# Kernel tuning notes

Hardware: AMD Instinct MI355X
Metric: run time of the kernel (lower is better)

Reference implementation:

```python
import jax, jax.numpy as jnp
import numpy as np
import math
from jax import lax

B, L, D, P, V, K = 4, 2048, 512, 128, 8, 4


def _lin(x, w, b):
    # torch Linear: y = x @ W^T + b, W shape (out, in)
    return jnp.einsum('...i,oi->...o', x, w) + b


def _gelu(v):
    return jax.nn.gelu(v, approximate=False)


def _dwconv_causal(x_ncl, w, b):
    # depthwise causal conv: torch Conv1d(groups=D, padding=K-1) then [:, :, :L]
    y = lax.conv_general_dilated(x_ncl, w, (1,), [(K - 1, 0)],
                                 dimension_numbers=('NCH', 'OIH', 'NCH'),
                                 feature_group_count=D)
    return y + b[None, :, None]


def _ln(v, g, b):
    m = v.mean(-1, keepdims=True)
    var = v.var(-1, keepdims=True)
    return (v - m) / jnp.sqrt(var + 1e-5) * g + b


def setup_inputs() -> dict:
    key = jax.random.key(0)
    it = iter(jax.random.split(key, 64))
    def nrm(shape, s=0.02):
        return jax.random.normal(next(it), shape, dtype=jnp.float32) * s
    z = lambda *s: jnp.zeros(s, jnp.float32)
    return dict(
        x=nrm((B, L, D), 1.0),
        lc_w=nrm((D, 1, K)), lc_b=z(D),
        cg_w=nrm((D, 1, K)), cg_b=z(D),
        cp_w=nrm((D, D)), cp_b=z(D),
        tw_w=nrm((D, D)), tw_b=z(D),
        omega_scale=jnp.full((D,), 0.01, jnp.float32),
        pi0_w=nrm((D, D)), pi0_b=z(D),
        pi2_w=nrm((D, D)), pi2_b=z(D),
        m1v_w=nrm((D, D)), m1v_b=z(D),
        m1o_w=nrm((D, D)), m1o_b=z(D),
        mag_w=nrm((D, D)), mag_b=z(D),
        mag_scale=jnp.asarray(5.0, jnp.float32),
        qo_w=nrm((D, D)), qo_b=z(D),
        ke_w=nrm((P, D)), ke_b=z(P),
        ve_w=nrm((V, D)), ve_b=z(V),
        sk0_w=nrm((D, 2 * D)), sk0_b=z(D),
        sk2_w=nrm((P, D)), sk2_b=z(P),
        sg_w=nrm((1, D)), sg_b=z(1),
        kvo_w=nrm((D, V)), kvo_b=z(D),
        ln_g=jnp.ones(5 * D, jnp.float32), ln_b=z(5 * D),
        o1_w=nrm((2 * D, 5 * D)), o1_b=z(2 * D),
        o2_w=nrm((D, 2 * D)), o2_b=z(D),
    )


def reference(x, lc_w, lc_b, cg_w, cg_b, cp_w, cp_b, tw_w, tw_b, omega_scale,
              pi0_w, pi0_b, pi2_w, pi2_b, m1v_w, m1v_b, m1o_w, m1o_b,
              mag_w, mag_b, mag_scale, qo_w, qo_b, ke_w, ke_b, ve_w, ve_b,
              sk0_w, sk0_b, sk2_w, sk2_b, sg_w, sg_b, kvo_w, kvo_b,
              ln_g, ln_b, o1_w, o1_b, o2_w, o2_b):
    Bs, Ls, Ds = x.shape
    # local gated causal depthwise conv branch
    xc = jnp.transpose(x, (0, 2, 1))                          # (B, D, L)
    co = _dwconv_causal(xc, lc_w, lc_b)
    cg = jax.nn.sigmoid(_dwconv_causal(xc, cg_w, cg_b))
    conv_out = _lin(jnp.transpose(co * cg, (0, 2, 1)), cp_w, cp_b)
    # evolving phases
    omega_scaled = _lin(x, tw_w, tw_b) * jnp.abs(omega_scale)
    phi = _lin(_gelu(_lin(x, pi0_w, pi0_b)), pi2_w, pi2_b) + jnp.cumsum(omega_scaled, axis=1)
    cos_phi = jnp.cos(phi)
    sin_phi = jnp.sin(phi)
    # magnitude-weighted phase memory
    v1 = _lin(x, m1v_w, m1v_b)
    magnitude = jax.nn.sigmoid(_lin(x, mag_w, mag_b)) * jnp.abs(mag_scale)
    wv1 = magnitude * v1
    sqrt_mag = jnp.sqrt(jnp.cumsum(magnitude, axis=1) + 1e-8)
    mem1_cos = jnp.cumsum(wv1 * cos_phi, axis=1) / sqrt_mag
    mem1_sin = jnp.cumsum(wv1 * sin_phi, axis=1) / sqrt_mag
    phi_q = phi + _lin(x, qo_w, qo_b)
    pos_ret = (mem1_cos * jnp.cos(phi_q) + mem1_sin * jnp.sin(phi_q)) / math.sqrt(Ds)
    pos_out = _lin(pos_ret, m1o_w, m1o_b)
    # phase-keyed associative KV memory
    query_phase = jnp.tanh(_lin(x, ke_w, ke_b)) * math.pi    # (B, L, P)
    values = _lin(x, ve_w, ve_b)                              # (B, L, V)
    store_gate = jax.nn.sigmoid(_lin(x, sg_w, sg_b))          # (B, L, 1)
    positions = jnp.arange(1, Ls + 1, dtype=x.dtype).reshape(1, -1, 1)
    context_avg = jnp.cumsum(x, axis=1) / positions
    storage_phase = jnp.tanh(_lin(_gelu(_lin(jnp.concatenate([x, context_avg], -1), sk0_w, sk0_b)), sk2_w, sk2_b)) * math.pi
    gated_vals = values * store_gate                          # (B, L, V)
    kv_mem_cos = jnp.cumsum(jnp.cos(storage_phase)[..., None] * gated_vals[:, :, None, :], axis=1)
    kv_mem_sin = jnp.cumsum(jnp.sin(storage_phase)[..., None] * gated_vals[:, :, None, :], axis=1)
    gate_norm = jnp.sqrt(jnp.maximum(jnp.cumsum(store_gate, axis=1), 1.0))[..., None]  # (B, L, 1, 1)
    kv_mem_cos = kv_mem_cos / gate_norm
    kv_mem_sin = kv_mem_sin / gate_norm
    kv_retrieved = (jnp.cos(query_phase)[..., None] * kv_mem_cos +
                    jnp.sin(query_phase)[..., None] * kv_mem_sin).sum(axis=2) / math.sqrt(P)
    kv_out = _lin(kv_retrieved, kvo_w, kvo_b)
    # combine (dropout is identity in eval)
    combined = jnp.concatenate([conv_out, pos_out, kv_out, x * cos_phi, x * sin_phi], axis=-1)
    h = _ln(combined, ln_g, ln_b)
    h = _lin(_gelu(_lin(h, o1_w, o1_b)), o2_w, o2_b)
    return x + h
```

## Files before the change

### kernel.cpp

```cpp
#include <hip/hip_runtime.h>
#include <cstdint>

typedef unsigned short u16;
typedef short short8 __attribute__((ext_vector_type(8)));
typedef float floatx4 __attribute__((ext_vector_type(4)));

#define B_ 4
#define L_ 2048
#define D_ 512
#define P_ 128
#define V_ 8
#define BL (B_ * L_)
#define NC_ 128
#define CH_ 16
#define PI_F 3.14159265358979323846f

__device__ inline u16 f2b(float f) {
    unsigned u = __float_as_uint(f);
    unsigned r = u + 0x7FFFu + ((u >> 16) & 1u);
    return (u16)(r >> 16);
}
__device__ inline float b2f(u16 h) {
    return __uint_as_float(((unsigned)h) << 16);
}
__device__ inline float gelu_f(float v) {
    return 0.5f * v * (1.0f + erff(v * 0.70710678118654752f));
}
__device__ inline float sigm(float v) {
    return 1.0f / (1.0f + __expf(-v));
}
__device__ inline float tanh_fast(float v) {
    return 1.0f - 2.0f / (1.0f + __expf(2.0f * v));
}

__device__ inline void async16(const u16* g, u16* l) {
    __builtin_amdgcn_global_load_lds(
        (const __attribute__((address_space(1))) unsigned int*)g,
        (__attribute__((address_space(3))) unsigned int*)l, 16, 0, 0);
}

extern __shared__ u16 smem_dyn[];

enum { EPI_F32 = 0, EPI_BF16 = 1, EPI_GELU_BF16 = 2, EPI_RESID_F32 = 3,
       EPI_PASS1 = 4, EPI_ATOMIC = 5 };

template <int EPI>
__device__ __forceinline__ void gemm_body(
    const u16* __restrict__ A, int lda,
    const u16* __restrict__ W, int ldw,
    const float* __restrict__ bias,
    void* __restrict__ Cout, int ldc, int N, int K,
    const float* __restrict__ resid, int mt, int nt)
{
    const int tid  = threadIdx.x;
    const int lane = tid & 63;
    const int wid  = tid >> 6;
    const int wm   = wid & 1, wn = wid >> 1;
    const int l16  = lane & 15, quad = lane >> 4;
    const int rswz = (l16 >> 1) & 3;

    floatx4 acc[4][4] = {};

    const u16* Ab = A + (size_t)(mt * 128) * lda;
    const u16* Wb = W + (size_t)(nt * 128) * ldw;

    const int srow = lane >> 2;
    const int scol = ((lane & 3) ^ ((srow >> 1) & 3)) * 8;
    const u16* ga0 = Ab + (size_t)(wid * 16 + srow) * lda + scol;
    const u16* ga1 = Ab + (size_t)(64 + wid * 16 + srow) * lda + scol;
    const u16* gb0 = Wb + (size_t)(wid * 16 + srow) * ldw + scol;
    const u16* gb1 = Wb + (size_t)(64 + wid * 16 + srow) * ldw + scol;

    const int lA0 = (wid * 16) * 32;
    const int lA1 = (64 + wid * 16) * 32;

    const int nsteps = K >> 5;

    auto stage = [&](int t, int s) {
        u16* base = smem_dyn + s * 8192;
        const int ko = t * 32;
        async16(ga0 + ko, base + lA0);
        async16(ga1 + ko, base + lA1);
        async16(gb0 + ko, base + 4096 + lA0);
        async16(gb1 + ko, base + 4096 + lA1);
    };

    auto readfrag = [&](int slot, short8 (&a)[4], short8 (&b)[4]) {
        const u16* As = smem_dyn + slot * 8192;
        const u16* Bs = As + 4096;
#pragma unroll
        for (int i = 0; i < 4; i++)
            a[i] = *(const short8*)(&As[(wm * 64 + i * 16 + l16) * 32 + (quad ^ rswz) * 8]);
#pragma unroll
        for (int j = 0; j < 4; j++)
            b[j] = *(const short8*)(&Bs[(wn * 64 + j * 16 + l16) * 32 + (quad ^ rswz) * 8]);
    };

    auto mfma16 = [&](short8 (&a)[4], short8 (&b)[4]) {
        __builtin_amdgcn_s_setprio(1);
#pragma unroll
        for (int i = 0; i < 4; i++)
#pragma unroll
            for (int j = 0; j < 4; j++)
                acc[i][j] = __builtin_amdgcn_mfma_f32_16x16x32_bf16(a[i], b[j], acc[i][j], 0, 0, 0);
        __builtin_amdgcn_s_setprio(0);
    };

    stage(0, 0);
    if (nsteps > 1) stage(1, 1);
    if (nsteps > 2) stage(2, 2);
    if (nsteps > 2)      asm volatile("s_waitcnt vmcnt(8)" ::: "memory");
    else if (nsteps > 1) asm volatile("s_waitcnt vmcnt(4)" ::: "memory");
    else                 asm volatile("s_waitcnt vmcnt(0)" ::: "memory");
    __builtin_amdgcn_s_barrier();
    asm volatile("" ::: "memory");

    short8 aE[4], bE[4], aO[4], bO[4];
    readfrag(0, aE, bE);

    for (int t = 0; t < nsteps; t += 2) {
        asm volatile("s_waitcnt lgkmcnt(0)" ::: "memory");
        if (t + 2 < nsteps)      asm volatile("s_waitcnt vmcnt(4)" ::: "memory");
        else if (t + 1 < nsteps) asm volatile("s_waitcnt vmcnt(0)" ::: "memory");
        __builtin_amdgcn_s_barrier();
        asm volatile("" ::: "memory");
        if (t + 3 < nsteps) stage(t + 3, t % 3);
        if (t + 1 < nsteps) readfrag((t + 1) % 3, aO, bO);
        mfma16(aE, bE);
        const int t1 = t + 1;
        asm volatile("s_waitcnt lgkmcnt(0)" ::: "memory");
        if (t1 + 2 < nsteps)      asm volatile("s_waitcnt vmcnt(4)" ::: "memory");
        else if (t1 + 1 < nsteps) asm volatile("s_waitcnt vmcnt(0)" ::: "memory");
        __builtin_amdgcn_s_barrier();
        asm volatile("" ::: "memory");
        if (t1 + 3 < nsteps) stage(t1 + 3, t1 % 3);
        if (t1 + 1 < nsteps) readfrag((t1 + 1) % 3, aE, bE);
        mfma16(aO, bO);
    }

#pragma unroll
    for (int i = 0; i < 4; i++) {
#pragma unroll
        for (int j = 0; j < 4; j++) {
#pragma unroll
            for (int r = 0; r < 4; r++) {
                int grow = mt * 128 + wm * 64 + i * 16 + quad * 4 + r;
                int gcol = nt * 128 + wn * 64 + j * 16 + l16;
                if (gcol < N) {
                    float v = acc[i][j][r] + (bias ? bias[gcol] : 0.0f);
                    size_t off = (size_t)grow * ldc + gcol;
                    if (EPI == EPI_F32)            ((float*)Cout)[off] = v;
                    else if (EPI == EPI_BF16)      ((u16*)Cout)[off] = f2b(v);
                    else if (EPI == EPI_GELU_BF16) ((u16*)Cout)[off] = f2b(gelu_f(v));
                    else if (EPI == EPI_PASS1) {
                        float vv = (gcol >= 512 && gcol < 1024) ? gelu_f(v) : v;
                        ((u16*)Cout)[off] = f2b(vv);
                    }
                    else if (EPI == EPI_RESID_F32) ((float*)Cout)[off] = v + resid[off];
                    else                           atomicAdd(&((float*)Cout)[off], v);
                }
            }
        }
    }
}

template <int EPI>
__global__ __launch_bounds__(256)
void gemm256(const u16* __restrict__ A, int lda,
             const u16* __restrict__ W, int ldw,
             const float* __restrict__ bias,
             void* __restrict__ C, int ldc, int N, int K,
             const float* __restrict__ resid)
{
    int kz = blockIdx.z;
    gemm_body<EPI>(A + (size_t)kz * K, lda, W + (size_t)kz * K, ldw,
                   kz == 0 ? bias : nullptr, C, ldc, N, K, resid,
                   blockIdx.x, blockIdx.y);
}

__global__ __launch_bounds__(256)
void mega1(const u16* __restrict__ xcat, const u16* __restrict__ convg,
           const u16* __restrict__ wcat1, const float* __restrict__ bcat1,
           const u16* __restrict__ kesgw, const float* __restrict__ kesgb,
           const u16* __restrict__ cpw, const float* __restrict__ cp_b,
           u16* __restrict__ out1, float* __restrict__ kesgo, u16* __restrict__ combined)
{
    int y = blockIdx.y, mt = blockIdx.x;
    if (y < 20)
        gemm_body<EPI_PASS1>(xcat, 1024, wcat1, 512, bcat1, out1, 2560, 2560, 512, nullptr, mt, y);
    else if (y < 22)
        gemm_body<EPI_F32>(xcat, 1024, kesgw, 512, kesgb, kesgo, 144, 144, 512, nullptr, mt, y - 20);
    else
        gemm_body<EPI_BF16>(convg, 512, cpw, 512, cp_b, combined, 2560, 512, 512, nullptr, mt, y - 22);
}

__global__ __launch_bounds__(256)
void mega2(const u16* __restrict__ posret, const u16* __restrict__ xcat,
           const u16* __restrict__ m1ow, const float* __restrict__ m1o_b,
           const u16* __restrict__ sk0w, const float* __restrict__ sk0_b,
           u16* __restrict__ combined, u16* __restrict__ sk0g)
{
    int y = blockIdx.y, mt = blockIdx.x;
    if (y < 4)
        gemm_body<EPI_BF16>(posret, 512, m1ow, 512, m1o_b, combined + 512, 2560, 512, 512, nullptr, mt, y);
    else
        gemm_body<EPI_GELU_BF16>(xcat, 1024, sk0w, 1024, sk0_b, sk0g, 512, 512, 1024, nullptr, mt, y - 4);
}

__global__ __launch_bounds__(256)
void prep_weights(const float* tw, const float* pi0, const float* m1v, const float* mag, const float* qo,
                  const float* ke, const float* ve, const float* sg,
                  const float* pi2, const float* cp, const float* sk0, const float* sk2,
                  const float* m1o, const float* o1, const float* o2,
                  const float* tw_b, const float* pi0_b, const float* m1v_b, const float* mag_b, const float* qo_b,
                  const float* ke_b, const float* ve_b, const float* sg_b,
                  u16* wcat1, float* bcat1, u16* kesgw, float* kesgb,
                  u16* pi2w, u16* cpw, u16* sk0w, u16* sk2w, u16* m1ow, u16* o1w, u16* o2w)
{
    int idx = blockIdx.x * 256 + threadIdx.x;
    const int n0 = 2560 * 512;
    const int n1 = n0 + 256 * 512;
    const int n2 = n1 + 512 * 512;
    const int n3 = n2 + 512 * 512;
    const int n4 = n3 + 512 * 1024;
    const int n5 = n4 + 128 * 512;
    const int n6 = n5 + 512 * 512;
    const int n7 = n6 + 1024 * 2560;
    const int n8 = n7 + 512 * 1024;
    const int n9 = n8 + 2560;
    const int n10 = n9 + 256;
    if (idx < n0) {
        int r = idx >> 9, k = idx & 511;
        const float* s = (r < 512) ? tw : (r < 1024) ? pi0 : (r < 1536) ? m1v : (r < 2048) ? mag : qo;
        wcat1[idx] = f2b(s[(r & 511) * 512 + k]);
    } else if (idx < n1) {
        int i = idx - n0; int r = i >> 9, k = i & 511;
        float v;
        if (r < 128)      v = ke[r * 512 + k];
        else if (r < 136) v = ve[(r - 128) * 512 + k];
        else if (r == 136) v = sg[k];
        else               v = 0.0f;
        kesgw[i] = f2b(v);
    }
    else if (idx < n2) { int i = idx - n1; pi2w[i] = f2b(pi2[i]); }
    else if (idx < n3) { int i = idx - n2; cpw[i]  = f2b(cp[i]); }
    else if (idx < n4) { int i = idx - n3; sk0w[i] = f2b(sk0[i]); }
    else if (idx < n5) { int i = idx - n4; sk2w[i] = f2b(sk2[i]); }
    else if (idx < n6) { int i = idx - n5; m1ow[i] = f2b(m1o[i]); }
    else if (idx < n7) { int i = idx - n6; o1w[i]  = f2b(o1[i]); }
    else if (idx < n8) { int i = idx - n7; o2w[i]  = f2b(o2[i]); }
    else if (idx < n9) {
        int i = idx - n8;
        const float* s = (i < 512) ? tw_b : (i < 1024) ? pi0_b : (i < 1536) ? m1v_b : (i < 2048) ? mag_b : qo_b;
        bcat1[i] = s[i & 511];
    } else if (idx < n10) {
        int i = idx - n9;
        kesgb[i] = (i < 128) ? ke_b[i] : (i < 136) ? ve_b[i - 128] : (i == 136) ? sg_b[0] : 0.0f;
    }
}

__global__ __launch_bounds__(256)
void conv_gate(const float* __restrict__ x,
               const float* __restrict__ lcw, const float* __restrict__ lcb,
               const float* __restrict__ cgw, const float* __restrict__ cgb,
               u16* __restrict__ out, u16* __restrict__ xcat)
{
    int idx = blockIdx.x * 256 + threadIdx.x;
    int d = idx & 511; int bl = idx >> 9;
    int l = bl & (L_ - 1); int b = bl >> 11;
    float a0 = 0.f, a1 = 0.f, xv3 = 0.f;
#pragma unroll
    for (int k = 0; k < 4; k++) {
        int ls = l - 3 + k;
        if (ls >= 0) {
            float xv = x[((size_t)(b * L_ + ls)) * 512 + d];
            if (k == 3) xv3 = xv;
            a0 += xv * lcw[d * 4 + k];
            a1 += xv * cgw[d * 4 + k];
        }
    }
    a0 += lcb[d];
    a1 = sigm(a1 + cgb[d]);
    out[idx] = f2b(a0 * a1);
    xcat[(size_t)bl * 1024 + d] = f2b(xv3);
}

__device__ __forceinline__ void scan_a_body(
    int blk, const u16* __restrict__ out1, const float* __restrict__ x,
    const float* __restrict__ oscale, const float* __restrict__ msc,
    float* __restrict__ cs_o, float* __restrict__ cs_x, float* __restrict__ cs_m)
{
    int nc = blk & 15, dt = (blk >> 4) & 7, b = blk >> 7;
    int t = threadIdx.x; int dl = t & 63, lg = t >> 6;
    int d = dt * 64 + dl;
    float os = fabsf(oscale[d]);
    float ms = fabsf(msc[0]);
    float so = 0.f, sx = 0.f, sm = 0.f;
    int l0 = nc * 128 + lg * 32;
    for (int i = 0; i < 32; i++) {
        size_t r = (size_t)(b * L_ + l0 + i);
        so += b2f(out1[r * 2560 + d]) * os;
        sm += sigm(b2f(out1[r * 2560 + 1536 + d])) * ms;
        sx += x[r * 512 + d];
    }
    __shared__ float sh[3][4][64];
    sh[0][lg][dl] = so; sh[1][lg][dl] = sx; sh[2][lg][dl] = sm;
    __syncthreads();
    if (t < 64) {
        float a = 0.f, xx = 0.f, m = 0.f;
        for (int g = 0; g < 4; g++) { a += sh[0][g][t]; xx += sh[1][g][t]; m += sh[2][g][t]; }
        size_t o = ((size_t)(b * 16 + nc)) * 512 + dt * 64 + t;
        cs_o[o] = a; cs_x[o] = xx; cs_m[o] = m;
    }
}

__device__ __forceinline__ void gate_body(const float* __restrict__ kesgo,
                                          float* __restrict__ gni)
{
    int b = threadIdx.x >> 6; int lane = threadIdx.x & 63;
    float v[32]; float s = 0.f;
#pragma unroll
    for (int i = 0; i < 32; i++) {
        int l = lane * 32 + i;
        v[i] = sigm(kesgo[((size_t)(b * L_ + l)) * 144 + 136]);
        s += v[i];
    }
    float sc = s;
#pragma unroll
    for (int ofs = 1; ofs < 64; ofs <<= 1) {
        float t = __shfl_up(sc, ofs, 64);
        if (lane >= ofs) sc += t;
    }
    float run = sc - s;
#pragma unroll
    for (int i = 0; i < 32; i++) {
        run += v[i];
        gni[b * L_ + lane * 32 + i] = rsqrtf(fmaxf(run, 1.0f));
    }
}

__global__ __launch_bounds__(256)
void stage2(const u16* __restrict__ out1, const u16* __restrict__ pi2w,
            const float* __restrict__ pi2_b, u16* __restrict__ phib,
            const float* __restrict__ x, const float* __restrict__ oscale,
            const float* __restrict__ msc,
            float* __restrict__ cs_o, float* __restrict__ cs_x, float* __restrict__ cs_m,
            const float* __restrict__ kesgo, float* __restrict__ gni)
{
    int blk = blockIdx.x;
    if (blk < 256)
        gemm_body<EPI_BF16>(out1 + 512, 2560, pi2w, 512, pi2_b, phib, 512, 512, 512,
                            nullptr, blk & 63, blk >> 6);
    else if (blk < 768)
        scan_a_body(blk - 256, out1, x, oscale, msc, cs_o, cs_x, cs_m);
    else
        gate_body(kesgo, gni);
}

__global__ __launch_bounds__(256)
void scan_c(const u16* __restrict__ out1, const u16* __restrict__ phib,
            const float* __restrict__ oscale, const float* __restrict__ msc,
            const float* __restrict__ cs_o,
            float* __restrict__ phi, float* __restrict__ cs_wc, float* __restrict__ cs_ws)
{
    int blk = blockIdx.x;
    int nc = blk & 15, dt = (blk >> 4) & 7, b = blk >> 7;
    int t = threadIdx.x; int dl = t & 63, lg = t >> 6;
    int d = dt * 64 + dl;
    float os = fabsf(oscale[d]);
    float ms = fabsf(msc[0]);
    int l0 = nc * 128 + lg * 32;
    float so = 0.f;
    for (int i = 0; i < 32; i++) {
        size_t r = (size_t)(b * L_ + l0 + i);
        so += b2f(out1[r * 2560 + d]) * os;
    }
    __shared__ float sh[4][64];
    __shared__ float shw[2][4][64];
    sh[lg][dl] = so;
    __syncthreads();
    float pre = 0.f;
    for (int p = 0; p < nc; p++) pre += cs_o[((size_t)(b * 16 + p)) * 512 + d];
    for (int g = 0; g < lg; g++) pre += sh[g][dl];
    float cum = pre, swc = 0.f, sws = 0.f;
    for (int i = 0; i < 32; i++) {
        size_t r = (size_t)(b * L_ + l0 + i);
        cum += b2f(out1[r * 2560 + d]) * os;
        float ph = b2f(phib[r * 512 + d]) + cum;
        phi[r * 512 + d] = ph;
        float mg = sigm(b2f(out1[r * 2560 + 1536 + d])) * ms;
        float wv = mg * b2f(out1[r * 2560 + 1024 + d]);
        float s = __sinf(ph), c = __cosf(ph);
        swc += wv * c; sws += wv * s;
    }
    shw[0][lg][dl] = swc; shw[1][lg][dl] = sws;
    __syncthreads();
    if (t < 64) {
        float a = 0.f, bb = 0.f;
        for (int g = 0; g < 4; g++) { a += shw[0][g][t]; bb += shw[1][g][t]; }
        size_t o = ((size_t)(b * 16 + nc)) * 512 + dt * 64 + t;
        cs_wc[o] = a; cs_ws[o] = bb;
    }
}

__global__ __launch_bounds__(256)
void scan_e(const u16* __restrict__ out1, const float* __restrict__ phi,
            const float* __restrict__ x, const float* __restrict__ msc,
            const float* __restrict__ cs_m, const float* __restrict__ cs_x,
            const float* __restrict__ cs_wc, const float* __restrict__ cs_ws,
            u16* __restrict__ posret, u16* __restrict__ xcat, u16* __restrict__ combined)
{
    int blk = blockIdx.x;
    int nc = blk & 15, dt = (blk >> 4) & 7, b = blk >> 7;
    int t = threadIdx.x; int dl = t & 63, lg = t >> 6;
    int d = dt * 64 + dl;
    float ms = fabsf(msc[0]);
    int l0 = nc * 128 + lg * 32;
    float sm = 0.f, swc = 0.f, sws = 0.f, sx = 0.f;
    for (int i = 0; i < 32; i++) {
        size_t r = (size_t)(b * L_ + l0 + i);
        float ph = phi[r * 512 + d];
        float mg = sigm(b2f(out1[r * 2560 + 1536 + d])) * ms;
        float wv = mg * b2f(out1[r * 2560 + 1024 + d]);
        float s = __sinf(ph), c = __cosf(ph);
        sm += mg; swc += wv * c; sws += wv * s; sx += x[r * 512 + d];
    }
    __shared__ float sh[4][4][64];
    sh[0][lg][dl] = sm; sh[1][lg][dl] = swc; sh[2][lg][dl] = sws; sh[3][lg][dl] = sx;
    __syncthreads();
    float cm = 0.f, cwc = 0.f, cws = 0.f, cx = 0.f;
    for (int p = 0; p < nc; p++) {
        size_t o = ((size_t)(b * 16 + p)) * 512 + d;
        cm += cs_m[o]; cwc += cs_wc[o]; cws += cs_ws[o]; cx += cs_x[o];
    }
    for (int g = 0; g < lg; g++) {
        cm += sh[0][g][dl]; cwc += sh[1][g][dl]; cws += sh[2][g][dl]; cx += sh[3][g][dl];
    }
    const float invsqD = 0.044194173824159216f;
    for (int i = 0; i < 32; i++) {
        int l = l0 + i;
        size_t r = (size_t)(b * L_ + l);
        float ph = phi[r * 512 + d];
        float mg = sigm(b2f(out1[r * 2560 + 1536 + d])) * ms;
        float wv = mg * b2f(out1[r * 2560 + 1024 + d]);
        float xv = x[r * 512 + d];
        float s = __sinf(ph), c = __cosf(ph);
        cm += mg; cwc += wv * c; cws += wv * s; cx += xv;
        float smag = sqrtf(cm + 1e-8f);
        float m1c = cwc / smag, m1s = cws / smag;
        float phq = ph + b2f(out1[r * 2560 + 2048 + d]);
        float sq = __sinf(phq), cq = __cosf(phq);
        float pr = (m1c * cq + m1s * sq) * invsqD;
        posret[r * 512 + d] = f2b(pr);
        xcat[r * 1024 + 512 + d] = f2b(cx / (float)(l + 1));
        combined[r * 2560 + 1536 + d] = f2b(xv * c);
        combined[r * 2560 + 2048 + d] = f2b(xv * s);
    }
}

__global__ __launch_bounds__(64)
void kv_chunk(const float* __restrict__ sppre, const float* __restrict__ kesgo,
              float* __restrict__ spc, float* __restrict__ sps,
              float* __restrict__ csum)
{
    int blk = blockIdx.x; int nc = blk & (NC_ - 1), b = blk >> 7;
    int t = threadIdx.x;
    float Sc[2][8] = {}, Ss[2][8] = {};
    for (int i = 0; i < CH_; i++) {
        size_t r = (size_t)(b * L_ + nc * CH_ + i);
        float sgate = sigm(kesgo[r * 144 + 136]);
        float g[8];
#pragma unroll
        for (int v = 0; v < 8; v++) g[v] = kesgo[r * 144 + 128 + v] * sgate;
#pragma unroll
        for (int j = 0; j < 2; j++) {
            int p = t + j * 64;
            float sp = tanh_fast(sppre[r * 128 + p]) * PI_F;
            float s = __sinf(sp), c = __cosf(sp);
            spc[r * 128 + p] = c; sps[r * 128 + p] = s;
#pragma unroll
            for (int v = 0; v < 8; v++) { Sc[j][v] += c * g[v]; Ss[j][v] += s * g[v]; }
        }
    }
    size_t base = (size_t)blk * 2048;
#pragma unroll
    for (int j = 0; j < 2; j++)
#pragma unroll
        for (int v = 0; v < 8; v++) {
            csum[base + (t + j * 64) * 8 + v]        = Sc[j][v];
            csum[base + 1024 + (t + j * 64) * 8 + v] = Ss[j][v];
        }
}

__global__ __launch_bounds__(256)
void kv_scan(const float* __restrict__ cin, float* __restrict__ cex)
{
    int t = blockIdx.x * 256 + threadIdx.x;
    int pv = t & 1023; int cs = (t >> 10) & 1; int b = t >> 11;
    float run = 0.f;
    for (int nc = 0; nc < NC_; nc++) {
        size_t o = ((size_t)(b * NC_ + nc)) * 2048 + cs * 1024 + pv;
        cex[o] = run; run += cin[o];
    }
}

__global__ __launch_bounds__(64)
void kv_retrieve(const float* __restrict__ spc, const float* __restrict__ sps,
                 const float* __restrict__ kesgo,
                 const float* __restrict__ gni, const float* __restrict__ cex,
                 const float* __restrict__ kvo_w, const float* __restrict__ kvo_b,
                 u16* __restrict__ combined)
{
    int blk = blockIdx.x; int nc = blk & (NC_ - 1), b = blk >> 7;
    int t = threadIdx.x;
    const int nb = t * 8;
    float wr[8][8], br[8];
#pragma unroll
    for (int n = 0; n < 8; n++) {
        *(float4*)&wr[n][0] = *(const float4*)&kvo_w[(nb + n) * 8];
        *(float4*)&wr[n][4] = *(const float4*)&kvo_w[(nb + n) * 8 + 4];
        br[n] = kvo_b[nb + n];
    }
    float Sc[2][8], Ss[2][8];
    size_t base = (size_t)blk * 2048;
#pragma unroll
    for (int j = 0; j < 2; j++)
#pragma unroll
        for (int v = 0; v < 8; v++) {
            Sc[j][v] = cex[base + (t + j * 64) * 8 + v];
            Ss[j][v] = cex[base + 1024 + (t + j * 64) * 8 + v];
        }
    for (int i = 0; i < CH_; i++) {
        size_t r = (size_t)(b * L_ + nc * CH_ + i);
        float sgate = sigm(kesgo[r * 144 + 136]);
        float g[8];
#pragma unroll
        for (int v = 0; v < 8; v++) g[v] = kesgo[r * 144 + 128 + v] * sgate;
        float part[8];
#pragma unroll
        for (int v = 0; v < 8; v++) part[v] = 0.f;
#pragma unroll
        for (int j = 0; j < 2; j++) {
            int p = t + j * 64;
            float c = spc[r * 128 + p], s = sps[r * 128 + p];
#pragma unroll
            for (int v = 0; v < 8; v++) { Sc[j][v] += c * g[v]; Ss[j][v] += s * g[v]; }
            float qp = tanh_fast(kesgo[r * 144 + p]) * PI_F;
            float sq = __sinf(qp), cq = __cosf(qp);
#pragma unroll
            for (int v = 0; v < 8; v++) part[v] += cq * Sc[j][v] + sq * Ss[j][v];
        }
#pragma unroll
        for (int ofs = 1; ofs < 64; ofs <<= 1)
#pragma unroll
            for (int v = 0; v < 8; v++) part[v] += __shfl_xor(part[v], ofs, 64);
        float scale = gni[r] * 0.08838834764831845f;
        float pv[8];
#pragma unroll
        for (int v = 0; v < 8; v++) pv[v] = part[v] * scale;
        u16 outv[8];
#pragma unroll
        for (int n = 0; n < 8; n++) {
            float a = br[n];
#pragma unroll
            for (int v = 0; v < 8; v++) a += pv[v] * wr[n][v];
            outv[n] = f2b(a);
        }
        *(uint4*)&combined[r * 2560 + 1024 + nb] = *(const uint4*)outv;
    }
}

__global__ __launch_bounds__(320)
void ln_rows(u16* __restrict__ combined, const float* __restrict__ g, const float* __restrict__ bb)
{
    size_t m = blockIdx.x; int t = threadIdx.x;
    u16 vv[8];
    *(uint4*)vv = *(const uint4*)&combined[m * 2560 + t * 8];
    float f[8]; float s = 0.f, s2 = 0.f;
#pragma unroll
    for (int k = 0; k < 8; k++) { f[k] = b2f(vv[k]); s += f[k]; s2 += f[k] * f[k]; }
#pragma unroll
    for (int ofs = 1; ofs < 64; ofs <<= 1) {
        s  += __shfl_xor(s, ofs, 64);
        s2 += __shfl_xor(s2, ofs, 64);
    }
    __shared__ float shs[5], shs2[5];
    int wv = t >> 6;
    if ((t & 63) == 0) { shs[wv] = s; shs2[wv] = s2; }
    __syncthreads();
    float S = 0.f, S2 = 0.f;
#pragma unroll
    for (int i = 0; i < 5; i++) { S += shs[i]; S2 += shs2[i]; }
    float mean = S * (1.0f / 2560.0f);
    float var  = S2 * (1.0f / 2560.0f) - mean * mean;
    float rstd = rsqrtf(var + 1e-5f);
#pragma unroll
    for (int k = 0; k < 8; k++) {
        int c = t * 8 + k;
        vv[k] = f2b((f[k] - mean) * rstd * g[c] + bb[c]);
    }
    *(uint4*)&combined[m * 2560 + t * 8] = *(const uint4*)vv;
}

extern "C" void kernel_launch(void* const* d_in, const int* in_sizes, int n_in,
                              void* d_out, int out_size, void* d_ws, size_t ws_size,
                              hipStream_t stream)
{
    const float* x     = (const float*)d_in[0];
    const float* lc_w  = (const float*)d_in[1];
    const float* lc_b  = (const float*)d_in[2];
    const float* cg_w  = (const float*)d_in[3];
    const float* cg_b  = (const float*)d_in[4];
    const float* cp_w  = (const float*)d_in[5];
    const float* cp_b  = (const float*)d_in[6];
    const float* tw_w  = (const float*)d_in[7];
    const float* tw_b  = (const float*)d_in[8];
    const float* omega_scale = (const float*)d_in[9];
    const float* pi0_w = (const float*)d_in[10];
    const float* pi0_b = (const float*)d_in[11];
    const float* pi2_w = (const float*)d_in[12];
    const float* pi2_b = (const float*)d_in[13];
    const float* m1v_w = (const float*)d_in[14];
    const float* m1v_b = (const float*)d_in[15];
    const float* m1o_w = (const float*)d_in[16];
    const float* m1o_b = (const float*)d_in[17];
    const float* mag_w = (const float*)d_in[18];
    const float* mag_b = (const float*)d_in[19];
    const float* mag_scale = (const float*)d_in[20];
    const float* qo_w  = (const float*)d_in[21];
    const float* qo_b  = (const float*)d_in[22];
    const float* ke_w  = (const float*)d_in[23];
    const float* ke_b  = (const float*)d_in[24];
    const float* ve_w  = (const float*)d_in[25];
    const float* ve_b  = (const float*)d_in[26];
    const float* sk0_w = (const float*)d_in[27];
    const float* sk0_b = (const float*)d_in[28];
    const float* sk2_w = (const float*)d_in[29];
    const float* sk2_b = (const float*)d_in[30];
    const float* sg_w  = (const float*)d_in[31];
    const float* sg_b  = (const float*)d_in[32];
    const float* kvo_w = (const float*)d_in[33];
    const float* kvo_b = (const float*)d_in[34];
    const float* ln_g  = (const float*)d_in[35];
    const float* ln_b  = (const float*)d_in[36];
    const float* o1_w  = (const float*)d_in[37];
    const float* o1_b  = (const float*)d_in[38];
    const float* o2_w  = (const float*)d_in[39];
    const float* o2_b  = (const float*)d_in[40];
    float* out = (float*)d_out;

    char* base = (char*)d_ws;
    size_t off = 0;
    auto alloc = [&](size_t bytes) -> void* {
        void* p = base + off;
        off += (bytes + 255) & ~(size_t)255;
        return p;
    };

    u16*   wcat1  = (u16*)  alloc((size_t)2560 * 512 * 2);
    float* bcat1  = (float*)alloc(2560 * 4);
    u16*   kesgw  = (u16*)  alloc((size_t)256 * 512 * 2);
    float* kesgb  = (float*)alloc(256 * 4);
    u16*   pi2w   = (u16*)  alloc((size_t)512 * 512 * 2);
    u16*   cpw    = (u16*)  alloc((size_t)512 * 512 * 2);
    u16*   sk0w   = (u16*)  alloc((size_t)512 * 1024 * 2);
    u16*   sk2w   = (u16*)  alloc((size_t)128 * 512 * 2);
    u16*   m1ow   = (u16*)  alloc((size_t)512 * 512 * 2);
    u16*   o1w    = (u16*)  alloc((size_t)1024 * 2560 * 2);
    u16*   o2w    = (u16*)  alloc((size_t)512 * 1024 * 2);
    u16*   xcat   = (u16*)  alloc((size_t)BL * 1024 * 2);
    u16*   out1   = (u16*)  alloc((size_t)BL * 2560 * 2);
    u16*   phib   = (u16*)  alloc((size_t)BL * 512 * 2);
    float* phi    = (float*)alloc((size_t)BL * 512 * 4);
    float* kesgo  = (float*)alloc((size_t)BL * 144 * 4);
    u16*   convg  = (u16*)  alloc((size_t)BL * 512 * 2);
    float* sppre  = (float*)alloc((size_t)BL * 128 * 4);
    u16*   combined = (u16*)alloc((size_t)BL * 2560 * 2);
    float* cs_o   = (float*)alloc((size_t)4 * 16 * 512 * 4);
    float* cs_x   = (float*)alloc((size_t)4 * 16 * 512 * 4);
    float* cs_m   = (float*)alloc((size_t)4 * 16 * 512 * 4);
    float* cs_wc  = (float*)alloc((size_t)4 * 16 * 512 * 4);
    float* cs_ws  = (float*)alloc((size_t)4 * 16 * 512 * 4);
    float* gni    = (float*)alloc((size_t)BL * 4);
    u16*   posret = convg;
    u16*   sk0g   = out1;
    float* spc    = phi;
    float* sps    = phi + (size_t)BL * 128;
    float* kvcs   = (float*)phib;
    float* kvex   = (float*)phib + (size_t)B_ * NC_ * 2048;
    u16*   o1g    = xcat;
    (void)ws_size; (void)in_sizes; (void)n_in; (void)out_size;

    const size_t SMEM = 49152;

    prep_weights<<<23307, 256, 0, stream>>>(
        tw_w, pi0_w, m1v_w, mag_w, qo_w, ke_w, ve_w, sg_w,
        pi2_w, cp_w, sk0_w, sk2_w, m1o_w, o1_w, o2_w,
        tw_b, pi0_b, m1v_b, mag_b, qo_b, ke_b, ve_b, sg_b,
        wcat1, bcat1, kesgw, kesgb, pi2w, cpw, sk0w, sk2w, m1ow, o1w, o2w);
    conv_gate<<<16384, 256, 0, stream>>>(x, lc_w, lc_b, cg_w, cg_b, convg, xcat);
    mega1<<<dim3(64, 26), 256, SMEM, stream>>>(xcat, convg, wcat1, bcat1,
                                               kesgw, kesgb, cpw, cp_b,
                                               out1, kesgo, combined);
    stage2<<<769, 256, SMEM, stream>>>(out1, pi2w, pi2_b, phib,
                                       x, omega_scale, mag_scale,
                                       cs_o, cs_x, cs_m, kesgo, gni);
    scan_c<<<512, 256, 0, stream>>>(out1, phib, omega_scale, mag_scale, cs_o,
                                    phi, cs_wc, cs_ws);
    scan_e<<<512, 256, 0, stream>>>(out1, phi, x, mag_scale, cs_m, cs_x, cs_wc, cs_ws,
                                    posret, xcat, combined);
    mega2<<<dim3(64, 8), 256, SMEM, stream>>>(posret, xcat, m1ow, m1o_b,
                                              sk0w, sk0_b, combined, sk0g);
    hipMemsetAsync(sppre, 0, (size_t)BL * 128 * 4, stream);
    gemm256<EPI_ATOMIC><<<dim3(64, 1, 4), 256, SMEM, stream>>>(sk0g, 512, sk2w, 512, sk2_b,
                                                               sppre, 128, 128, 128, nullptr);
    kv_chunk<<<4 * NC_, 64, 0, stream>>>(sppre, kesgo, spc, sps, kvcs);
    kv_scan<<<32, 256, 0, stream>>>(kvcs, kvex);
    kv_retrieve<<<4 * NC_, 64, 0, stream>>>(spc, sps, kesgo, gni, kvex, kvo_w, kvo_b, combined);
    ln_rows<<<8192, 320, 0, stream>>>(combined, ln_g, ln_b);
    gemm256<EPI_GELU_BF16><<<dim3(64, 8), 256, SMEM, stream>>>(combined, 2560, o1w, 2560, o1_b,
                                                               o1g, 1024, 1024, 2560, nullptr);
    gemm256<EPI_RESID_F32><<<dim3(64, 4), 256, SMEM, stream>>>(o1g, 1024, o2w, 1024, o2_b,
                                                               out, 512, 512, 1024, x);
}
```

Measured before the change: 560.4 us.

## Give each wave private LDS A tiles and load B fragments directly from global

Restructures the GEMM main loop so each wave stages only its own 64-row A slice into a private triple-buffered LDS region, while the weight (B) fragments are read straight from global memory into registers. This drops the workgroup-wide s_barrier calls between pipeline steps, since no LDS is shared across waves anymore. In exchange, A rows shared by waves with the same wm are loaded twice, and B is fetched from global/L2 with per-lane strided loads instead of coalesced shared staging. The vmcnt accounting now mixes async LDS loads with register loads, which adds ordering risk.

```diff
diff --git a/kernel.cpp b/kernel.cpp
--- a/kernel.cpp
+++ b/kernel.cpp
@@ -61,41 +61,44 @@
 
     floatx4 acc[4][4] = {};
 
-    const u16* Ab = A + (size_t)(mt * 128) * lda;
-    const u16* Wb = W + (size_t)(nt * 128) * ldw;
+    const u16* Ab = A + (size_t)(mt * 128 + wm * 64) * lda;
+    const u16* Wb = W + (size_t)(nt * 128 + wn * 64) * ldw;
 
     const int srow = lane >> 2;
     const int scol = ((lane & 3) ^ ((srow >> 1) & 3)) * 8;
-    const u16* ga0 = Ab + (size_t)(wid * 16 + srow) * lda + scol;
-    const u16* ga1 = Ab + (size_t)(64 + wid * 16 + srow) * lda + scol;
-    const u16* gb0 = Wb + (size_t)(wid * 16 + srow) * ldw + scol;
-    const u16* gb1 = Wb + (size_t)(64 + wid * 16 + srow) * ldw + scol;
-
-    const int lA0 = (wid * 16) * 32;
-    const int lA1 = (64 + wid * 16) * 32;
-
+    const u16* gA0 = Ab + (size_t)(srow)      * lda + scol;
+    const u16* gA1 = Ab + (size_t)(16 + srow) * lda + scol;
+    const u16* gA2 = Ab + (size_t)(32 + srow) * lda + scol;
+    const u16* gA3 = Ab + (size_t)(48 + srow) * lda + scol;
+    const u16* gB0 = Wb + (size_t)(l16)      * ldw + quad * 8;
+    const u16* gB1 = Wb + (size_t)(16 + l16) * ldw + quad * 8;
+    const u16* gB2 = Wb + (size_t)(32 + l16) * ldw + quad * 8;
+    const u16* gB3 = Wb + (size_t)(48 + l16) * ldw + quad * 8;
+
+    u16* wbase = smem_dyn + wid * (3 * 2048);
     const int nsteps = K >> 5;
 
-    auto stage = [&](int t, int s) {
-        u16* base = smem_dyn + s * 8192;
+    auto stageA = [&](int t, int s) {
+        u16* dst = wbase + s * 2048;
         const int ko = t * 32;
-        async16(ga0 + ko, base + lA0);
-        async16(ga1 + ko, base + lA1);
-        async16(gb0 + ko, base + 4096 + lA0);
-        async16(gb1 + ko, base + 4096 + lA1);
+        async16(gA0 + ko, dst);
+        async16(gA1 + ko, dst + 512);
+        async16(gA2 + ko, dst + 1024);
+        async16(gA3 + ko, dst + 1536);
     };
-
-    auto readfrag = [&](int slot, short8 (&a)[4], short8 (&b)[4]) {
-        const u16* As = smem_dyn + slot * 8192;
-        const u16* Bs = As + 4096;
+    auto loadB = [&](int t, short8 (&b)[4]) {
+        const int ko = t * 32;
+        b[0] = *(const short8*)(gB0 + ko);
+        b[1] = *(const short8*)(gB1 + ko);
+        b[2] = *(const short8*)(gB2 + ko);
+        b[3] = *(const short8*)(gB3 + ko);
+    };
+    auto readA = [&](int slot, short8 (&a)[4]) {
+        const u16* s = wbase + slot * 2048;
 #pragma unroll
         for (int i = 0; i < 4; i++)
-            a[i] = *(const short8*)(&As[(wm * 64 + i * 16 + l16) * 32 + (quad ^ rswz) * 8]);
-#pragma unroll
-        for (int j = 0; j < 4; j++)
-            b[j] = *(const short8*)(&Bs[(wn * 64 + j * 16 + l16) * 32 + (quad ^ rswz) * 8]);
+            a[i] = *(const short8*)(&s[(i * 16 + l16) * 32 + (quad ^ rswz) * 8]);
     };
-
     auto mfma16 = [&](short8 (&a)[4], short8 (&b)[4]) {
         __builtin_amdgcn_s_setprio(1);
 #pragma unroll
@@ -106,35 +109,30 @@
         __builtin_amdgcn_s_setprio(0);
     };
 
-    stage(0, 0);
-    if (nsteps > 1) stage(1, 1);
-    if (nsteps > 2) stage(2, 2);
-    if (nsteps > 2)      asm volatile("s_waitcnt vmcnt(8)" ::: "memory");
-    else if (nsteps > 1) asm volatile("s_waitcnt vmcnt(4)" ::: "memory");
-    else                 asm volatile("s_waitcnt vmcnt(0)" ::: "memory");
-    __builtin_amdgcn_s_barrier();
-    asm volatile("" ::: "memory");
-
     short8 aE[4], bE[4], aO[4], bO[4];
-    readfrag(0, aE, bE);
+
+    stageA(0, 0);
+    loadB(0, bE);
+    stageA(1, 1);
+    stageA(2, 2);
+    asm volatile("s_waitcnt vmcnt(12)" ::: "memory");
+    readA(0, aE);
 
     for (int t = 0; t < nsteps; t += 2) {
+        if (t + 2 < nsteps) asm volatile("s_waitcnt vmcnt(4)" ::: "memory");
+        else                asm volatile("s_waitcnt vmcnt(0)" ::: "memory");
         asm volatile("s_waitcnt lgkmcnt(0)" ::: "memory");
-        if (t + 2 < nsteps)      asm volatile("s_waitcnt vmcnt(4)" ::: "memory");
-        else if (t + 1 < nsteps) asm volatile("s_waitcnt vmcnt(0)" ::: "memory");
-        __builtin_amdgcn_s_barrier();
-        asm volatile("" ::: "memory");
-        if (t + 3 < nsteps) stage(t + 3, t % 3);
-        if (t + 1 < nsteps) readfrag((t + 1) % 3, aO, bO);
+        if (t + 1 < nsteps) loadB(t + 1, bO);
+        if (t + 3 < nsteps) stageA(t + 3, t % 3);
+        if (t + 1 < nsteps) readA((t + 1) % 3, aO);
         mfma16(aE, bE);
         const int t1 = t + 1;
+        if (t1 + 2 < nsteps) asm volatile("s_waitcnt vmcnt(4)" ::: "memory");
+        else                 asm volatile("s_waitcnt vmcnt(0)" ::: "memory");
         asm volatile("s_waitcnt lgkmcnt(0)" ::: "memory");
-        if (t1 + 2 < nsteps)      asm volatile("s_waitcnt vmcnt(4)" ::: "memory");
-        else if (t1 + 1 < nsteps) asm volatile("s_waitcnt vmcnt(0)" ::: "memory");
-        __builtin_amdgcn_s_barrier();
-        asm volatile("" ::: "memory");
-        if (t1 + 3 < nsteps) stage(t1 + 3, t1 % 3);
-        if (t1 + 1 < nsteps) readfrag((t1 + 1) % 3, aE, bE);
+        if (t1 + 1 < nsteps) loadB(t1 + 1, bE);
+        if (t1 + 3 < nsteps) stageA(t1 + 3, t1 % 3);
+        if (t1 + 1 < nsteps) readA((t1 + 1) % 3, aE);
         mfma16(aO, bO);
     }
 
```

Result: slower. 675.4 us (+20.5%).
